# Kernel optimization log

Measured on AMD Instinct MI355X. Metric: run time of the kernel, lower is better.

Reference implementation:

```python
import jax, jax.numpy as jnp
import numpy as np


def _gcn_conv(h, src, dst, W, b, n):
    # PyG GCNConv: x @ W, then symmetric-normalized aggregation with self-loops
    deg = jax.ops.segment_sum(jnp.ones(src.shape[0], h.dtype), dst, num_segments=n)
    dinv = jax.lax.rsqrt(jnp.maximum(deg, 1.0))  # deg >= 1 because self-loops are included
    norm = dinv[src] * dinv[dst]                 # [E]
    m = (h @ W)[src] * norm[:, None]             # gather + scale
    return jax.ops.segment_sum(m, dst, num_segments=n) + b


def setup_inputs() -> dict:
    key = jax.random.key(0)
    N, E, F, H, L, V = 50000, 800000, 128, 256, 64, 128
    ks = jax.random.split(key, 16)
    s = lambda fan_in: 1.0 / np.sqrt(fan_in)
    return {
        "x": jax.random.randint(ks[0], (N,), 0, V),
        "edge_index": jax.random.randint(ks[1], (2, E), 0, N),
        "eps": jax.random.normal(ks[2], (N, L), jnp.float32),
        "emb": jax.random.normal(ks[3], (V, F), jnp.float32),
        "W1": jax.random.normal(ks[4], (F, H), jnp.float32) * s(F),
        "b1": jnp.zeros((H,), jnp.float32),
        "W2": jax.random.normal(ks[5], (H, H), jnp.float32) * s(H),
        "b2": jnp.zeros((H,), jnp.float32),
        "Wmu": jax.random.normal(ks[6], (H, L), jnp.float32) * s(H),
        "bmu": jnp.zeros((L,), jnp.float32),
        "Wlv": jax.random.normal(ks[7], (H, L), jnp.float32) * s(H),
        "blv": jnp.zeros((L,), jnp.float32),
        "W3": jax.random.normal(ks[8], (L, H), jnp.float32) * s(L),
        "b3": jnp.zeros((H,), jnp.float32),
        "W4": jax.random.normal(ks[9], (H, V), jnp.float32) * s(H),
        "b4": jnp.zeros((V,), jnp.float32),
        "Wcap": jax.random.normal(ks[10], (L, 1), jnp.float32) * s(L),
        "bcap": jnp.zeros((1,), jnp.float32),
    }


def reference(x, edge_index, eps, emb, W1, b1, W2, b2, Wmu, bmu, Wlv, blv, W3, b3, W4, b4, Wcap, bcap):
    n = x.shape[0]
    loops = jnp.arange(n, dtype=edge_index.dtype)
    src = jnp.concatenate([edge_index[0], loops])  # add self-loops once, reuse
    dst = jnp.concatenate([edge_index[1], loops])

    h = emb[x]                                      # [N, F] embedding lookup
    h = jax.nn.relu(_gcn_conv(h, src, dst, W1, b1, n))
    h = jax.nn.relu(_gcn_conv(h, src, dst, W2, b2, n))
    mu = h @ Wmu + bmu
    logvar = h @ Wlv + blv
    z = mu + eps * jnp.exp(0.5 * logvar)            # reparameterize
    recon_x = jax.nn.relu(z @ W3 + b3) @ W4 + b4    # decode
    capitalize = jax.nn.sigmoid(z @ Wcap + bcap)
    return recon_x, capitalize, mu, logvar
```

## Files before the change

### kernel.cpp

```cpp
#include <hip/hip_runtime.h>
#include <math.h>


typedef __attribute__((ext_vector_type(8))) short bf16x8;
typedef __attribute__((ext_vector_type(8))) unsigned short u16x8;
typedef __attribute__((ext_vector_type(4))) float f32x4;

__device__ inline unsigned short f2bf(float x) {
    unsigned u = __float_as_uint(x);
    return (unsigned short)((u + 0x7FFFu + ((u >> 16) & 1u)) >> 16);
}
__device__ inline float bf2f(unsigned short h) {
    return __uint_as_float(((unsigned)h) << 16);
}

__global__ __launch_bounds__(256) void k_deg_count(const int* __restrict__ dst,
                                                   int* __restrict__ degint, int E) {
    int e = blockIdx.x * 256 + threadIdx.x;
    if (e < E) atomicAdd(&degint[dst[e]], 1);
}

#define SCAN_BLOCK 1024
__global__ __launch_bounds__(SCAN_BLOCK) void k_scan_local(
        const int* __restrict__ degint, int* __restrict__ row_ptr,
        int* __restrict__ bsum, float* __restrict__ dinv, int N) {
    __shared__ int s[SCAN_BLOCK];
    int gid = blockIdx.x * SCAN_BLOCK + threadIdx.x;
    int d = (gid < N) ? (degint[gid] + 1) : 0;
    if (gid < N) dinv[gid] = rsqrtf((float)d);
    s[threadIdx.x] = d;
    __syncthreads();
    for (int off = 1; off < SCAN_BLOCK; off <<= 1) {
        int t = (threadIdx.x >= off) ? s[threadIdx.x - off] : 0;
        __syncthreads();
        s[threadIdx.x] += t;
        __syncthreads();
    }
    if (gid < N) row_ptr[gid] = s[threadIdx.x] - d;
    if (threadIdx.x == SCAN_BLOCK - 1) bsum[blockIdx.x] = s[SCAN_BLOCK - 1];
}

__global__ __launch_bounds__(256) void k_scan_add(int* __restrict__ row_ptr,
                                                  const int* __restrict__ bsum,
                                                  int N, int T) {
    const int gid = blockIdx.x * 256 + threadIdx.x;
    const int myb = (blockIdx.x * 256) / SCAN_BLOCK;
    const int lane = threadIdx.x & 63;
    int v = (lane < myb) ? bsum[lane] : 0;
    v += __shfl_xor(v, 1, 64);
    v += __shfl_xor(v, 2, 64);
    v += __shfl_xor(v, 4, 64);
    v += __shfl_xor(v, 8, 64);
    v += __shfl_xor(v, 16, 64);
    v += __shfl_xor(v, 32, 64);
    if (gid < N) row_ptr[gid] += v;
    if (gid == 0) row_ptr[N] = T;
}

__global__ __launch_bounds__(256) void k_fill(
        const int* __restrict__ src, const int* __restrict__ dst,
        const int* __restrict__ x, const float* __restrict__ dinv,
        const int* __restrict__ row_ptr, int* __restrict__ cursor,
        int4* __restrict__ pack, int E, int N) {
    const int base = (blockIdx.x * 256 + threadIdx.x) * 4;
#pragma unroll
    for (int j = 0; j < 4; ++j) {
        int e = base + j;
        if (e < E) {
            int s = src[e], d = dst[e];
            float w = dinv[s] * dinv[d];
            int pos = row_ptr[d] + atomicAdd(&cursor[d], 1);
            pack[pos] = make_int4(__float_as_int(w), s, x[s], 0);
        } else if (e < E + N) {
            int i = e - E;
            float di = dinv[i];
            int pos = row_ptr[i] + atomicAdd(&cursor[i], 1);
            pack[pos] = make_int4(__float_as_int(di * di), i, x[i], 0);
        }
    }
}

__global__ __launch_bounds__(256) void k_prep(
        const float* __restrict__ B0, unsigned short* __restrict__ h0, int K0, int N0,
        const float* __restrict__ B1, unsigned short* __restrict__ h1, int K1, int N1,
        const float* __restrict__ B2, unsigned short* __restrict__ h2, int K2, int N2,
        const float* __restrict__ B3, unsigned short* __restrict__ h3, int K3, int N3,
        const float* __restrict__ B4, unsigned short* __restrict__ h4, int K4, int N4,
        const float* __restrict__ emb, const float* __restrict__ W1,
        unsigned short* __restrict__ tabT, int Mt, int Kt, int Nt) {
    __shared__ float As[16][64];
    __shared__ float Bs[16][64];
    const int tid = threadIdx.x;

    if (blockIdx.y < 5) {
        const float* B; unsigned short* Bh; int K, Ncol;
        switch (blockIdx.y) {
            case 0: B = B0; Bh = h0; K = K0; Ncol = N0; break;
            case 1: B = B1; Bh = h1; K = K1; Ncol = N1; break;
            case 2: B = B2; Bh = h2; K = K2; Ncol = N2; break;
            case 3: B = B3; Bh = h3; K = K3; Ncol = N3; break;
            default: B = B4; Bh = h4; K = K4; Ncol = N4; break;
        }
        int i = blockIdx.x * 256 + tid;
        if (i < K * Ncol) {
            int k = i / Ncol, n = i - k * Ncol;
            Bh[(long)n * K + k] = f2bf(B[i]);
        }
        return;
    }

    if (blockIdx.x >= 8) return;
    constexpr int BM = 64, BN = 64, BK = 16;
    const int tx = tid & 15, ty = tid >> 4;
    const int rowBase = (blockIdx.x & 1) * BM;
    const int colBase = (blockIdx.x >> 1) * BN;
    const int lr = tid >> 2, lc4 = tid & 3;
    const int br = tid >> 4, bc4 = tid & 15;
    const int arow = rowBase + lr;
    const int Ktq = Kt >> 2, Ntq = Nt >> 2;
    const float4* A4 = (const float4*)emb;
    const float4* B4v = (const float4*)W1;
    float acc[4][4] = {{0.f}};
    for (int k0 = 0; k0 < Kt; k0 += BK) {
        float4 av = make_float4(0.f, 0.f, 0.f, 0.f);
        if (arow < Mt) av = A4[(long)arow * Ktq + (k0 >> 2) + lc4];
        As[lc4 * 4 + 0][lr] = av.x;
        As[lc4 * 4 + 1][lr] = av.y;
        As[lc4 * 4 + 2][lr] = av.z;
        As[lc4 * 4 + 3][lr] = av.w;
        float4 bv = B4v[(long)(k0 + br) * Ntq + (colBase >> 2) + bc4];
        *(float4*)&Bs[br][bc4 * 4] = bv;
        __syncthreads();
#pragma unroll
        for (int k = 0; k < BK; ++k) {
            float4 a4v = *(const float4*)&As[k][ty * 4];
            float4 b4v = *(const float4*)&Bs[k][tx * 4];
            float aa[4] = {a4v.x, a4v.y, a4v.z, a4v.w};
            float bb[4] = {b4v.x, b4v.y, b4v.z, b4v.w};
#pragma unroll
            for (int i = 0; i < 4; ++i)
#pragma unroll
                for (int j = 0; j < 4; ++j)
                    acc[i][j] = fmaf(aa[i], bb[j], acc[i][j]);
        }
        __syncthreads();
    }
#pragma unroll
    for (int i = 0; i < 4; ++i) {
        int row = rowBase + ty * 4 + i;
        if (row < Mt) {
#pragma unroll
            for (int c = 0; c < 4; ++c) {
                int col = colBase + tx * 4 + c;
                tabT[(long)col * Mt + row] = f2bf(acc[i][c]);
            }
        }
    }
}

__global__ __launch_bounds__(256) void k_coef(
        const int4* __restrict__ pack, const int* __restrict__ row_ptr,
        unsigned short* __restrict__ cb, int N) {
    const int wave = threadIdx.x >> 6;
    const int lane = threadIdx.x & 63;
    const int node = blockIdx.x * 4 + wave;
    if (node >= N) return;
    const int tok0 = lane, tok1 = lane + 64;
    float c0 = 0.f, c1 = 0.f;
    const int beg = row_ptr[node], end = row_ptr[node + 1];
    int e = beg;
    for (; e + 4 <= end; e += 4) {
        int4 p0 = pack[e];
        int4 p1 = pack[e + 1];
        int4 p2 = pack[e + 2];
        int4 p3 = pack[e + 3];
        c0 += (p0.z == tok0) ? __int_as_float(p0.x) : 0.f;
        c1 += (p0.z == tok1) ? __int_as_float(p0.x) : 0.f;
        c0 += (p1.z == tok0) ? __int_as_float(p1.x) : 0.f;
        c1 += (p1.z == tok1) ? __int_as_float(p1.x) : 0.f;
        c0 += (p2.z == tok0) ? __int_as_float(p2.x) : 0.f;
        c1 += (p2.z == tok1) ? __int_as_float(p2.x) : 0.f;
        c0 += (p3.z == tok0) ? __int_as_float(p3.x) : 0.f;
        c1 += (p3.z == tok1) ? __int_as_float(p3.x) : 0.f;
    }
    for (; e < end; ++e) {
        int4 p = pack[e];
        c0 += (p.z == tok0) ? __int_as_float(p.x) : 0.f;
        c1 += (p.z == tok1) ? __int_as_float(p.x) : 0.f;
    }
    const long base = (long)node * 128;
    cb[base + lane]      = f2bf(c0);
    cb[base + lane + 64] = f2bf(c1);
}

template<bool RELU>
__global__ __launch_bounds__(256) void k_gemm_bn128(
        const unsigned short* __restrict__ A, const unsigned short* __restrict__ Bt,
        const float* __restrict__ bias, unsigned short* __restrict__ Cb,
        int M, int K, int Ncol) {
    __shared__ unsigned short Ash[64][72];
    __shared__ unsigned short Bsh[128][72];
    const int tid = threadIdx.x;
    const int lane = tid & 63, w = tid >> 6;
    const int fr = lane & 15, quad = lane >> 4;
    const int wm0 = w * 16;
    const int rowBase = blockIdx.x * 64;
    const int colBase = blockIdx.y * 128;

    const int arow = tid >> 2;
    const int aseg = (tid & 3) << 4;
    int agrow = rowBase + arow; if (agrow >= M) agrow = M - 1;
    const long abase = (long)agrow * K + aseg;
    const int brow = tid >> 1;
    const int bseg = (tid & 1) << 5;
    const long bbase = (long)(colBase + brow) * K + bseg;

    f32x4 acc[8];
#pragma unroll
    for (int j = 0; j < 8; ++j) acc[j] = (f32x4){0.f, 0.f, 0.f, 0.f};

    for (int k0 = 0; k0 < K; k0 += 64) {
        *(bf16x8*)&Ash[arow][aseg]      = *(const bf16x8*)&A[abase + k0];
        *(bf16x8*)&Ash[arow][aseg + 8]  = *(const bf16x8*)&A[abase + k0 + 8];
        *(bf16x8*)&Bsh[brow][bseg]      = *(const bf16x8*)&Bt[bbase + k0];
        *(bf16x8*)&Bsh[brow][bseg + 8]  = *(const bf16x8*)&Bt[bbase + k0 + 8];
        *(bf16x8*)&Bsh[brow][bseg + 16] = *(const bf16x8*)&Bt[bbase + k0 + 16];
        *(bf16x8*)&Bsh[brow][bseg + 24] = *(const bf16x8*)&Bt[bbase + k0 + 24];
        __syncthreads();
        bf16x8 af0 = *(const bf16x8*)&Ash[wm0 + fr][quad * 8];
        bf16x8 af1 = *(const bf16x8*)&Ash[wm0 + fr][32 + quad * 8];
#pragma unroll
        for (int j = 0; j < 8; ++j) {
            bf16x8 b0 = *(const bf16x8*)&Bsh[j * 16 + fr][quad * 8];
            acc[j] = __builtin_amdgcn_mfma_f32_16x16x32_bf16(af0, b0, acc[j], 0, 0, 0);
        }
#pragma unroll
        for (int j = 0; j < 8; ++j) {
            bf16x8 b1 = *(const bf16x8*)&Bsh[j * 16 + fr][32 + quad * 8];
            acc[j] = __builtin_amdgcn_mfma_f32_16x16x32_bf16(af1, b1, acc[j], 0, 0, 0);
        }
        __syncthreads();
    }

#pragma unroll
    for (int j = 0; j < 8; ++j) {
        const int col = colBase + j * 16 + fr;
        const float bv = bias[col];
#pragma unroll
        for (int r = 0; r < 4; ++r) {
            const int row = rowBase + wm0 + quad * 4 + r;
            if (row < M) {
                float v = acc[j][r] + bv;
                if (RELU) v = fmaxf(v, 0.f);
                Cb[(long)row * Ncol + col] = f2bf(v);
            }
        }
    }
}

__global__ __launch_bounds__(256) void k_gemm_tail(
        const unsigned short* __restrict__ A, const unsigned short* __restrict__ Wml,
        const unsigned short* __restrict__ W3t, const unsigned short* __restrict__ W4t,
        const float* __restrict__ bmu, const float* __restrict__ blv,
        const float* __restrict__ eps, const float* __restrict__ Wcap,
        const float* __restrict__ bcap, const float* __restrict__ b3,
        const float* __restrict__ b4, float* __restrict__ mu,
        float* __restrict__ lv, float* __restrict__ recon,
        float* __restrict__ cap, int M) {
    constexpr int K = 256;
    __shared__ __align__(16) char smem[54272];
    unsigned short (*Bsh)[40] = (unsigned short (*)[40])smem;
    unsigned short (*Ash)[40] = (unsigned short (*)[40])(smem + 20480);
    unsigned short (*Zs)[72]  = (unsigned short (*)[72])(smem + 25600);
    unsigned short (*Ts)[264] = (unsigned short (*)[264])(smem + 20480);
    const int tid = threadIdx.x;
    const int lane = tid & 63, w = tid >> 6;
    const int fr = lane & 15, quad = lane >> 4;
    const int wm0 = w * 16;
    const int rowBase = blockIdx.x * 64;

    {
        const int zr = tid >> 2, zc = (tid & 3) * 18;
#pragma unroll
        for (int c = 0; c < 18; ++c) Zs[zr][zc + c] = 0;
    }

    const int arow = tid >> 2;
    const int aseg = (tid & 3) << 3;
    int agrow = rowBase + arow; if (agrow >= M) agrow = M - 1;
    const long abase = (long)agrow * K + aseg;
    const int brow = tid >> 1;
    const int bseg = (tid & 1) << 4;
    const long bbase = (long)brow * K + bseg;

    f32x4 acc[8];
#pragma unroll
    for (int j = 0; j < 8; ++j) acc[j] = (f32x4){0.f, 0.f, 0.f, 0.f};

    for (int k0 = 0; k0 < K; k0 += 32) {
        *(bf16x8*)&Ash[arow][aseg]     = *(const bf16x8*)&A[abase + k0];
        *(bf16x8*)&Bsh[brow][bseg]     = *(const bf16x8*)&Wml[bbase + k0];
        *(bf16x8*)&Bsh[brow][bseg + 8] = *(const bf16x8*)&Wml[bbase + k0 + 8];
        __syncthreads();
        bf16x8 ahf = *(const bf16x8*)&Ash[wm0 + fr][quad * 8];
#pragma unroll
        for (int j = 0; j < 8; ++j) {
            bf16x8 bhf = *(const bf16x8*)&Bsh[j * 16 + fr][quad * 8];
            acc[j] = __builtin_amdgcn_mfma_f32_16x16x32_bf16(ahf, bhf, acc[j], 0, 0, 0);
        }
        __syncthreads();
    }

    float capacc[4] = {0.f, 0.f, 0.f, 0.f};
#pragma unroll
    for (int j = 0; j < 4; ++j) {
        const int c = j * 16 + fr;
        const float bm = bmu[c], bl = blv[c];
        const float wc = Wcap[c];
#pragma unroll
        for (int r = 0; r < 4; ++r) {
            const int rl = wm0 + quad * 4 + r;
            const int row = rowBase + rl;
            if (row < M) {
                const long o = (long)row * 64 + c;
                float mv = acc[j][r] + bm;
                float lvv = acc[j + 4][r] + bl;
                mu[o] = mv;
                lv[o] = lvv;
                float zz = fmaf(eps[o], expf(0.5f * lvv), mv);
                Zs[rl][c] = f2bf(zz);
                capacc[r] = fmaf(zz, wc, capacc[r]);
            }
        }
    }
    const float b0 = bcap[0];
#pragma unroll
    for (int r = 0; r < 4; ++r) {
        float v = capacc[r];
        v += __shfl_xor(v, 1, 64);
        v += __shfl_xor(v, 2, 64);
        v += __shfl_xor(v, 4, 64);
        v += __shfl_xor(v, 8, 64);
        if (fr == 0) {
            const int row = rowBase + wm0 + quad * 4 + r;
            if (row < M) cap[row] = 1.f / (1.f + expf(-(v + b0)));
        }
    }

    f32x4 acc1[16];
#pragma unroll
    for (int j = 0; j < 16; ++j) acc1[j] = (f32x4){0.f, 0.f, 0.f, 0.f};
    for (int k0 = 0; k0 < 64; k0 += 32) {
        {
            const long wb = (long)tid * 64 + k0;
            *(bf16x8*)&Bsh[tid][0]  = *(const bf16x8*)&W3t[wb];
            *(bf16x8*)&Bsh[tid][8]  = *(const bf16x8*)&W3t[wb + 8];
            *(bf16x8*)&Bsh[tid][16] = *(const bf16x8*)&W3t[wb + 16];
            *(bf16x8*)&Bsh[tid][24] = *(const bf16x8*)&W3t[wb + 24];
        }
        __syncthreads();
        bf16x8 af = *(const bf16x8*)&Zs[wm0 + fr][k0 + quad * 8];
#pragma unroll
        for (int j = 0; j < 16; ++j) {
            bf16x8 bf = *(const bf16x8*)&Bsh[j * 16 + fr][quad * 8];
            acc1[j] = __builtin_amdgcn_mfma_f32_16x16x32_bf16(af, bf, acc1[j], 0, 0, 0);
        }
        __syncthreads();
    }

#pragma unroll
    for (int j = 0; j < 16; ++j) {
        const int col = j * 16 + fr;
        const float bv = b3[col];
#pragma unroll
        for (int r = 0; r < 4; ++r) {
            const int rl = wm0 + quad * 4 + r;
            Ts[rl][col] = f2bf(fmaxf(acc1[j][r] + bv, 0.f));
        }
    }
    __syncthreads();

    f32x4 acc2[8];
#pragma unroll
    for (int j = 0; j < 8; ++j) acc2[j] = (f32x4){0.f, 0.f, 0.f, 0.f};
    const int br2 = tid >> 1;
    const int bs2 = (tid & 1) << 4;
    for (int k0 = 0; k0 < 256; k0 += 32) {
        const long wb = (long)br2 * 256 + k0 + bs2;
        *(bf16x8*)&Bsh[br2][bs2]     = *(const bf16x8*)&W4t[wb];
        *(bf16x8*)&Bsh[br2][bs2 + 8] = *(const bf16x8*)&W4t[wb + 8];
        __syncthreads();
        bf16x8 at = *(const bf16x8*)&Ts[wm0 + fr][k0 + quad * 8];
#pragma unroll
        for (int j = 0; j < 8; ++j) {
            bf16x8 bf = *(const bf16x8*)&Bsh[j * 16 + fr][quad * 8];
            acc2[j] = __builtin_amdgcn_mfma_f32_16x16x32_bf16(at, bf, acc2[j], 0, 0, 0);
        }
        __syncthreads();
    }

#pragma unroll
    for (int j = 0; j < 8; ++j) {
        const int col = j * 16 + fr;
        const float bv = b4[col];
#pragma unroll
        for (int r = 0; r < 4; ++r) {
            const int row = rowBase + wm0 + quad * 4 + r;
            if (row < M) recon[(long)row * 128 + col] = acc2[j][r] + bv;
        }
    }
}

__global__ __launch_bounds__(256) void k_agg_nb(
        const unsigned short* __restrict__ h1, const int* __restrict__ row_ptr,
        const int2* __restrict__ pk2, unsigned short* __restrict__ Ob, int N) {
    const int wave = threadIdx.x >> 6;
    const int lane = threadIdx.x & 63;
    const int node = blockIdx.x * 4 + wave;
    if (node >= N) return;
    const int half = lane >> 5;
    const int col  = lane & 31;
    const u16x8* hrow = (const u16x8*)h1;
    float acc[8] = {0.f, 0.f, 0.f, 0.f, 0.f, 0.f, 0.f, 0.f};
    const int beg = row_ptr[node], end = row_ptr[node + 1];
    int e = beg;
    for (; e + 8 <= end; e += 8) {
        int2 q0 = pk2[2 * (e + 0 + half)];
        int2 q1 = pk2[2 * (e + 2 + half)];
        int2 q2 = pk2[2 * (e + 4 + half)];
        int2 q3 = pk2[2 * (e + 6 + half)];
        u16x8 v0 = hrow[(long)q0.y * 32 + col];
        u16x8 v1 = hrow[(long)q1.y * 32 + col];
        u16x8 v2 = hrow[(long)q2.y * 32 + col];
        u16x8 v3 = hrow[(long)q3.y * 32 + col];
        float w0 = __int_as_float(q0.x), w1 = __int_as_float(q1.x);
        float w2 = __int_as_float(q2.x), w3 = __int_as_float(q3.x);
#pragma unroll
        for (int c = 0; c < 8; ++c) {
            acc[c] = fmaf(bf2f(v0[c]), w0, acc[c]);
            acc[c] = fmaf(bf2f(v1[c]), w1, acc[c]);
            acc[c] = fmaf(bf2f(v2[c]), w2, acc[c]);
            acc[c] = fmaf(bf2f(v3[c]), w3, acc[c]);
        }
    }
    for (; e + 2 <= end; e += 2) {
        int2 q = pk2[2 * (e + half)];
        float w = __int_as_float(q.x);
        u16x8 v = hrow[(long)q.y * 32 + col];
#pragma unroll
        for (int c = 0; c < 8; ++c) acc[c] = fmaf(bf2f(v[c]), w, acc[c]);
    }
    if (e < end) {
        int2 q = pk2[2 * e];
        float w = (half == 0) ? __int_as_float(q.x) : 0.f;
        u16x8 v = hrow[(long)q.y * 32 + col];
#pragma unroll
        for (int c = 0; c < 8; ++c) acc[c] = fmaf(bf2f(v[c]), w, acc[c]);
    }
#pragma unroll
    for (int c = 0; c < 8; ++c) acc[c] += __shfl_xor(acc[c], 32, 64);
    if (lane < 32) {
        u16x8 o;
#pragma unroll
        for (int c = 0; c < 8; ++c) o[c] = f2bf(acc[c]);
        ((u16x8*)Ob)[(long)node * 32 + col] = o;
    }
}

extern "C" void kernel_launch(void* const* d_in, const int* in_sizes, int n_in,
                              void* d_out, int out_size, void* d_ws, size_t ws_size,
                              hipStream_t stream) {
    const int*   x    = (const int*)d_in[0];
    const int*   ei   = (const int*)d_in[1];
    const float* eps  = (const float*)d_in[2];
    const float* emb  = (const float*)d_in[3];
    const float* W1   = (const float*)d_in[4];
    const float* b1   = (const float*)d_in[5];
    const float* W2   = (const float*)d_in[6];
    const float* b2   = (const float*)d_in[7];
    const float* Wmu  = (const float*)d_in[8];
    const float* bmu  = (const float*)d_in[9];
    const float* Wlv  = (const float*)d_in[10];
    const float* blv  = (const float*)d_in[11];
    const float* W3   = (const float*)d_in[12];
    const float* b3   = (const float*)d_in[13];
    const float* W4   = (const float*)d_in[14];
    const float* b4   = (const float*)d_in[15];
    const float* Wcap = (const float*)d_in[16];
    const float* bcap = (const float*)d_in[17];

    const int N = in_sizes[0];
    const int E = in_sizes[1] / 2;
    const int H = in_sizes[5];
    const int L = in_sizes[9];
    const int V = in_sizes[15];
    const int F = in_sizes[4] / H;
    const int T = E + N;

    const int* src = ei;
    const int* dst = ei + E;

    char* w = (char*)d_ws;
    unsigned short* h1b  = (unsigned short*)w; w += (size_t)N * H * 2;
    unsigned short* a2b  = (unsigned short*)w; w += (size_t)N * H * 2;
    unsigned short* h2b  = (unsigned short*)w; w += (size_t)N * H * 2;
    unsigned short* cb   = (unsigned short*)w; w += (size_t)N * V * 2;
    int*   degint = (int*)w;   w += (size_t)N * 4;
    int*   cursor = (int*)w;   w += (size_t)N * 4;
    int*   rowp   = (int*)w;   w += (size_t)(N + 1) * 4;
    float* dinv   = (float*)w; w += (size_t)N * 4;
    int*   bsum   = (int*)w;   w += 256 * 4;
    int4*  pack   = (int4*)w;  w += (size_t)T * 16;
    unsigned short* tabT = (unsigned short*)w; w += (size_t)H * V * 2;
    unsigned short* W2t  = (unsigned short*)w; w += (size_t)H * H * 2;
    unsigned short* Wml  = (unsigned short*)w; w += (size_t)H * 2 * L * 2;
    unsigned short* W3t  = (unsigned short*)w; w += (size_t)L * H * 2;
    unsigned short* W4t  = (unsigned short*)w; w += (size_t)H * V * 2;

    float* outp    = (float*)d_out;
    float* recon   = outp;
    float* cap     = outp + (size_t)N * V;
    float* mu      = outp + (size_t)N * V + N;
    float* logvar  = mu + (size_t)N * L;

    const int nN  = (N + 255) / 256;
    const int nE  = (E + 255) / 256;
    const int nT4 = (T + 1023) / 1024;
    const int nSc = (N + SCAN_BLOCK - 1) / SCAN_BLOCK;
    const int gM64 = (N + 63) / 64;

    hipMemsetAsync(degint, 0, (size_t)N * 8, stream);
    k_deg_count<<<nE, 256, 0, stream>>>(dst, degint, E);
    k_scan_local<<<nSc, SCAN_BLOCK, 0, stream>>>(degint, rowp, bsum, dinv, N);
    k_scan_add<<<nN, 256, 0, stream>>>(rowp, bsum, N, T);
    k_fill<<<nT4, 256, 0, stream>>>(src, dst, x, dinv, rowp, cursor, pack, E, N);

    unsigned short* WmlLo = Wml;
    unsigned short* WmlHi = Wml + (size_t)L * H;
    k_prep<<<dim3((H * H + 255) / 256, 6), 256, 0, stream>>>(
        W2, W2t, H, H,
        Wmu, WmlLo, H, L,
        Wlv, WmlHi, H, L,
        W3, W3t, L, H,
        W4, W4t, H, V,
        emb, W1, tabT, V, F, H);

    k_coef<<<(N + 3) / 4, 256, 0, stream>>>(pack, rowp, cb, N);
    k_gemm_bn128<true><<<dim3(gM64, H / 128), 256, 0, stream>>>(
        cb, tabT, b1, h1b, N, V, H);

    k_agg_nb<<<(N + 3) / 4, 256, 0, stream>>>(h1b, rowp, (const int2*)pack, a2b, N);
    k_gemm_bn128<true><<<dim3(gM64, H / 128), 256, 0, stream>>>(
        a2b, W2t, b2, h2b, N, H, H);

    k_gemm_tail<<<gM64, 256, 0, stream>>>(
        h2b, Wml, W3t, W4t, bmu, blv, eps, Wcap, bcap, b3, b4,
        mu, logvar, recon, cap, N);
}
```

Measured before the change: 389.0 us.

## Replace token-coefficient GEMM with direct gather of precomputed emb@W1 rows

The first GCN layer used to build a per-node token coefficient matrix (N x V), then multiply it by a transposed emb@W1 table with a GEMM. Now the table is stored row-major (V x H) and each node directly gathers and accumulates the weighted table rows of its neighbours' tokens, fusing bias and ReLU. This drops the coefficient buffer write and read and one GEMM launch, at the cost of random 512-byte gathers per edge from a small table that should stay cache-resident.

After: 388.8 us. Within noise of the previous version (-0.0%).

```diff
diff --git a/kernel.cpp b/kernel.cpp
--- a/kernel.cpp
+++ b/kernel.cpp
@@ -87,7 +87,7 @@
         const float* __restrict__ B3, unsigned short* __restrict__ h3, int K3, int N3,
         const float* __restrict__ B4, unsigned short* __restrict__ h4, int K4, int N4,
         const float* __restrict__ emb, const float* __restrict__ W1,
-        unsigned short* __restrict__ tabT, int Mt, int Kt, int Nt) {
+        unsigned short* __restrict__ tab, int Mt, int Kt, int Nt) {
     __shared__ float As[16][64];
     __shared__ float Bs[16][64];
     const int tid = threadIdx.x;
@@ -152,45 +152,56 @@
 #pragma unroll
             for (int c = 0; c < 4; ++c) {
                 int col = colBase + tx * 4 + c;
-                tabT[(long)col * Mt + row] = f2bf(acc[i][c]);
+                tab[(long)row * Nt + col] = f2bf(acc[i][c]);
             }
         }
     }
 }
 
-__global__ __launch_bounds__(256) void k_coef(
+__global__ __launch_bounds__(256) void k_conv1_gather(
         const int4* __restrict__ pack, const int* __restrict__ row_ptr,
-        unsigned short* __restrict__ cb, int N) {
+        const unsigned short* __restrict__ tab, const float* __restrict__ b1,
+        unsigned short* __restrict__ h1, int N) {
     const int wave = threadIdx.x >> 6;
     const int lane = threadIdx.x & 63;
     const int node = blockIdx.x * 4 + wave;
     if (node >= N) return;
-    const int tok0 = lane, tok1 = lane + 64;
-    float c0 = 0.f, c1 = 0.f;
+    const ushort4* t4 = (const ushort4*)tab;
+    const float4 bv = ((const float4*)b1)[lane];
+    float a0 = 0.f, a1 = 0.f, a2 = 0.f, a3 = 0.f;
     const int beg = row_ptr[node], end = row_ptr[node + 1];
     int e = beg;
     for (; e + 4 <= end; e += 4) {
-        int4 p0 = pack[e];
-        int4 p1 = pack[e + 1];
-        int4 p2 = pack[e + 2];
-        int4 p3 = pack[e + 3];
-        c0 += (p0.z == tok0) ? __int_as_float(p0.x) : 0.f;
-        c1 += (p0.z == tok1) ? __int_as_float(p0.x) : 0.f;
-        c0 += (p1.z == tok0) ? __int_as_float(p1.x) : 0.f;
-        c1 += (p1.z == tok1) ? __int_as_float(p1.x) : 0.f;
-        c0 += (p2.z == tok0) ? __int_as_float(p2.x) : 0.f;
-        c1 += (p2.z == tok1) ? __int_as_float(p2.x) : 0.f;
-        c0 += (p3.z == tok0) ? __int_as_float(p3.x) : 0.f;
-        c1 += (p3.z == tok1) ? __int_as_float(p3.x) : 0.f;
+        int4 p0 = pack[e],     p1 = pack[e + 1];
+        int4 p2 = pack[e + 2], p3 = pack[e + 3];
+        ushort4 v0 = t4[(long)p0.z * 64 + lane];
+        ushort4 v1 = t4[(long)p1.z * 64 + lane];
+        ushort4 v2 = t4[(long)p2.z * 64 + lane];
+        ushort4 v3 = t4[(long)p3.z * 64 + lane];
+        float w0 = __int_as_float(p0.x), w1 = __int_as_float(p1.x);
+        float w2 = __int_as_float(p2.x), w3 = __int_as_float(p3.x);
+        a0 = fmaf(bf2f(v0.x), w0, a0); a1 = fmaf(bf2f(v0.y), w0, a1);
+        a2 = fmaf(bf2f(v0.z), w0, a2); a3 = fmaf(bf2f(v0.w), w0, a3);
+        a0 = fmaf(bf2f(v1.x), w1, a0); a1 = fmaf(bf2f(v1.y), w1, a1);
+        a2 = fmaf(bf2f(v1.z), w1, a2); a3 = fmaf(bf2f(v1.w), w1, a3);
+        a0 = fmaf(bf2f(v2.x), w2, a0); a1 = fmaf(bf2f(v2.y), w2, a1);
+        a2 = fmaf(bf2f(v2.z), w2, a2); a3 = fmaf(bf2f(v2.w), w2, a3);
+        a0 = fmaf(bf2f(v3.x), w3, a0); a1 = fmaf(bf2f(v3.y), w3, a1);
+        a2 = fmaf(bf2f(v3.z), w3, a2); a3 = fmaf(bf2f(v3.w), w3, a3);
     }
     for (; e < end; ++e) {
         int4 p = pack[e];
-        c0 += (p.z == tok0) ? __int_as_float(p.x) : 0.f;
-        c1 += (p.z == tok1) ? __int_as_float(p.x) : 0.f;
-    }
-    const long base = (long)node * 128;
-    cb[base + lane]      = f2bf(c0);
-    cb[base + lane + 64] = f2bf(c1);
+        float w = __int_as_float(p.x);
+        ushort4 v = t4[(long)p.z * 64 + lane];
+        a0 = fmaf(bf2f(v.x), w, a0); a1 = fmaf(bf2f(v.y), w, a1);
+        a2 = fmaf(bf2f(v.z), w, a2); a3 = fmaf(bf2f(v.w), w, a3);
+    }
+    ushort4 o;
+    o.x = f2bf(fmaxf(a0 + bv.x, 0.f));
+    o.y = f2bf(fmaxf(a1 + bv.y, 0.f));
+    o.z = f2bf(fmaxf(a2 + bv.z, 0.f));
+    o.w = f2bf(fmaxf(a3 + bv.w, 0.f));
+    ((ushort4*)h1)[(long)node * 64 + lane] = o;
 }
 
 template<bool RELU>
@@ -504,14 +515,13 @@
     unsigned short* h1b  = (unsigned short*)w; w += (size_t)N * H * 2;
     unsigned short* a2b  = (unsigned short*)w; w += (size_t)N * H * 2;
     unsigned short* h2b  = (unsigned short*)w; w += (size_t)N * H * 2;
-    unsigned short* cb   = (unsigned short*)w; w += (size_t)N * V * 2;
     int*   degint = (int*)w;   w += (size_t)N * 4;
     int*   cursor = (int*)w;   w += (size_t)N * 4;
     int*   rowp   = (int*)w;   w += (size_t)(N + 1) * 4;
     float* dinv   = (float*)w; w += (size_t)N * 4;
     int*   bsum   = (int*)w;   w += 256 * 4;
     int4*  pack   = (int4*)w;  w += (size_t)T * 16;
-    unsigned short* tabT = (unsigned short*)w; w += (size_t)H * V * 2;
+    unsigned short* tab  = (unsigned short*)w; w += (size_t)V * H * 2;
     unsigned short* W2t  = (unsigned short*)w; w += (size_t)H * H * 2;
     unsigned short* Wml  = (unsigned short*)w; w += (size_t)H * 2 * L * 2;
     unsigned short* W3t  = (unsigned short*)w; w += (size_t)L * H * 2;
@@ -543,11 +553,9 @@
         Wlv, WmlHi, H, L,
         W3, W3t, L, H,
         W4, W4t, H, V,
-        emb, W1, tabT, V, F, H);
-
-    k_coef<<<(N + 3) / 4, 256, 0, stream>>>(pack, rowp, cb, N);
-    k_gemm_bn128<true><<<dim3(gM64, H / 128), 256, 0, stream>>>(
-        cb, tabT, b1, h1b, N, V, H);
+        emb, W1, tab, V, F, H);
+
+    k_conv1_gather<<<(N + 3) / 4, 256, 0, stream>>>(pack, rowp, tab, b1, h1b, N);
 
     k_agg_nb<<<(N + 3) / 4, 256, 0, stream>>>(h1b, rowp, (const int2*)pack, a2b, N);
     k_gemm_bn128<true><<<dim3(gM64, H / 128), 256, 0, stream>>>(
```
